# Performance work log

Hardware: AMD Instinct MI355X
Metric: run time of the kernel (lower is better)

Reference implementation:

```python
import jax, jax.numpy as jnp
import numpy as np

N_SRC, N_TGT, E = 50000, 10000, 150000
D_IN, D_OUT = 512, 512
N_ETYPES, N_NTYPES = 8, 4


def setup_inputs() -> dict:
    key = jax.random.key(0)
    ks = jax.random.split(key, 9)
    scale = 1.0 / np.sqrt(D_IN)
    return {
        "x_src": jax.random.normal(ks[0], (N_SRC, D_IN), jnp.float32),
        "x_target": jax.random.normal(ks[1], (N_TGT, D_IN), jnp.float32),
        "rel_W": jax.random.normal(ks[2], (N_ETYPES, D_IN, D_OUT), jnp.float32) * scale,
        "root_W": jax.random.normal(ks[3], (N_NTYPES, D_IN, D_OUT), jnp.float32) * scale,
        "root_b": jax.random.normal(ks[4], (N_NTYPES, D_OUT), jnp.float32) * scale,
        "edge_src": jax.random.randint(ks[5], (E,), 0, N_SRC, jnp.int64).astype(jnp.int32),
        "edge_dst": jax.random.randint(ks[6], (E,), 0, N_TGT, jnp.int64).astype(jnp.int32),
        "edge_type": jax.random.randint(ks[7], (E,), 0, N_ETYPES, jnp.int64).astype(jnp.int32),
        "target_node_type": jax.random.randint(ks[8], (N_TGT,), 0, N_NTYPES, jnp.int64).astype(jnp.int32),
    }


def reference(x_src, x_target, rel_W, root_W, root_b,
              edge_src, edge_dst, edge_type, target_node_type):
    T = rel_W.shape[0]
    n_tgt = x_target.shape[0]
    # Transform every source node under every relation (grouped GEMM),
    # then gather per edge: msg_e = W_{etype_e} @ x_src[src_e].
    h = jnp.einsum('ni,tio->tno', x_src, rel_W)          # [T, N_src, D_out]
    msg = h[edge_type, edge_src]                          # [E, D_out]
    # PyG aggr='mean' is applied per edge type then SUMMED across types:
    # segment-mean keyed by (dst, etype), empty segments contribute 0.
    seg = edge_dst * T + edge_type                        # [E]
    sums = jax.ops.segment_sum(msg, seg, num_segments=n_tgt * T)
    counts = jax.ops.segment_sum(jnp.ones((msg.shape[0],), msg.dtype), seg,
                                 num_segments=n_tgt * T)
    means = sums / jnp.maximum(counts, 1.0)[:, None]      # [N_tgt*T, D_out]
    out = means.reshape(n_tgt, T, -1).sum(axis=1)         # [N_tgt, D_out]
    # Per-node-type root linear (with bias), selected per target node.
    root = jnp.einsum('ni,tio->nto', x_target, root_W) + root_b[None]  # [N_tgt, NT, D_out]
    root_sel = jnp.take_along_axis(root, target_node_type[:, None, None], axis=1)[:, 0]
    return out + root_sel
```

## Files before the change

kernel.cpp:

```cpp
#include <hip/hip_runtime.h>
#include <hip/hip_bf16.h>

#define D 512
#define T_ETYPES 8
#define NT_TYPES 4
#define K_MAIN 4096
#define K_A 4608
#define K_B 6144
#define SPLITS 6
#define KSPLIT 768
#define BK 64


typedef __attribute__((ext_vector_type(8))) short bf16x8;
typedef __attribute__((ext_vector_type(4))) float f32x4;

__device__ __forceinline__ unsigned short f2bf(float f) {
    union { float f; unsigned u; } u{f};
    unsigned r = u.u + 0x7FFF + ((u.u >> 16) & 1);
    return (unsigned short)(r >> 16);
}
__device__ __forceinline__ float bf2f(unsigned short h) {
    union { unsigned u; float f; } v{(unsigned)h << 16};
    return v.f;
}

__device__ __forceinline__ void gl16(const unsigned short* g, unsigned short* l) {
    __builtin_amdgcn_global_load_lds(
        (const __attribute__((address_space(1))) unsigned int*)g,
        (__attribute__((address_space(3))) unsigned int*)l,
        16, 0, 0);
}

__global__ void convert_xsrc(const float* __restrict__ x, unsigned short* __restrict__ xb,
                             int n8) {
    int stride = gridDim.x * 256;
    for (int i = blockIdx.x * 256 + threadIdx.x; i < n8; i += stride) {
        const float4* p = reinterpret_cast<const float4*>(x + (size_t)i * 8);
        float4 v0 = p[0], v1 = p[1];
        uint4 u;
        u.x = (unsigned)f2bf(v0.x) | ((unsigned)f2bf(v0.y) << 16);
        u.y = (unsigned)f2bf(v0.z) | ((unsigned)f2bf(v0.w) << 16);
        u.z = (unsigned)f2bf(v1.x) | ((unsigned)f2bf(v1.y) << 16);
        u.w = (unsigned)f2bf(v1.z) | ((unsigned)f2bf(v1.w) << 16);
        reinterpret_cast<uint4*>(xb)[i] = u;
    }
}

__global__ void convert_weights(const float* __restrict__ relW,
                                const float* __restrict__ rootW,
                                unsigned short* __restrict__ WbT) {
    __shared__ float tile[32][33];
    int c0 = blockIdx.x * 32;
    int o0 = blockIdx.y * 32;
    int tid = threadIdx.x;
#pragma unroll
    for (int it = 0; it < 4; ++it) {
        int idx = it * 256 + tid;
        int oc = idx & 31, cc = idx >> 5;
        int c = c0 + cc, o = o0 + oc;
        float v = (c < K_MAIN) ? relW[(size_t)c * D + o]
                               : rootW[(size_t)(c - K_MAIN) * D + o];
        tile[cc][oc] = v;
    }
    __syncthreads();
#pragma unroll
    for (int it = 0; it < 4; ++it) {
        int idx = it * 256 + tid;
        int cc = idx & 31, oc = idx >> 5;
        int o = o0 + oc, c = c0 + cc;
        int csw = (c & ~63) | (((((c >> 3) & 7) ^ (o & 7))) << 3) | (c & 7);
        WbT[(size_t)o * K_B + csw] = f2bf(tile[cc][oc]);
    }
}

__global__ void hist_kernel(const int* __restrict__ edst, const int* __restrict__ etyp,
                            int* __restrict__ counts, int E) {
    int e = blockIdx.x * 256 + threadIdx.x;
    if (e < E) atomicAdd(&counts[edst[e] * T_ETYPES + etyp[e]], 1);
}

__global__ void scan1(const int* __restrict__ counts, int* __restrict__ partial,
                      int* __restrict__ blockSums, int n) {
    __shared__ int sh[256];
    int tid = threadIdx.x, i = blockIdx.x * 256 + tid;
    int c = (i < n) ? counts[i] : 0;
    int val = c;
    sh[tid] = val; __syncthreads();
#pragma unroll
    for (int off = 1; off < 256; off <<= 1) {
        int add = (tid >= off) ? sh[tid - off] : 0;
        __syncthreads();
        val += add; sh[tid] = val;
        __syncthreads();
    }
    if (i < n) partial[i] = val - c;
    if (tid == 255) blockSums[blockIdx.x] = val;
}

__global__ void scan2(int* __restrict__ blockSums, int nb) {
    __shared__ int sh[512];
    int tid = threadIdx.x;
    int c = (tid < nb) ? blockSums[tid] : 0;
    int val = c;
    sh[tid] = val; __syncthreads();
#pragma unroll
    for (int off = 1; off < 512; off <<= 1) {
        int add = (tid >= off) ? sh[tid - off] : 0;
        __syncthreads();
        val += add; sh[tid] = val;
        __syncthreads();
    }
    if (tid < nb) blockSums[tid] = val - c;
}

__global__ void scan3(const int* __restrict__ partial, const int* __restrict__ blockSums,
                      int* __restrict__ offsets, int* __restrict__ cursors, int n, int E) {
    int i = blockIdx.x * 256 + threadIdx.x;
    if (i < n) {
        int v = partial[i] + blockSums[i >> 8];
        offsets[i] = v;
        cursors[i] = v;
    }
    if (i == 0) offsets[n] = E;
}

__global__ void scatter_kernel(const int* __restrict__ esrc, const int* __restrict__ edst,
                               const int* __restrict__ etyp, int* __restrict__ cursors,
                               int* __restrict__ perm, int E) {
    int e = blockIdx.x * 256 + threadIdx.x;
    if (e < E) {
        int seg = edst[e] * T_ETYPES + etyp[e];
        int pos = atomicAdd(&cursors[seg], 1);
        perm[pos] = esrc[e];
    }
}

__global__ void thist2(const int* __restrict__ tnt, int* __restrict__ bcnt, int M) {
    __shared__ int h[NT_TYPES];
    if (threadIdx.x < NT_TYPES) h[threadIdx.x] = 0;
    __syncthreads();
    int i = blockIdx.x * 256 + threadIdx.x;
    if (i < M) atomicAdd(&h[tnt[i]], 1);
    __syncthreads();
    if (threadIdx.x < NT_TYPES) bcnt[blockIdx.x * NT_TYPES + threadIdx.x] = h[threadIdx.x];
}

__global__ void tprep2(const int* __restrict__ bcnt, int nb,
                       int* __restrict__ boff, int* __restrict__ gstart,
                       int* __restrict__ endv) {
    __shared__ int sb[128 * NT_TYPES];
    __shared__ int gs[NT_TYPES];
    int tid = threadIdx.x;
    for (int i = tid; i < nb * NT_TYPES; i += blockDim.x) sb[i] = bcnt[i];
    __syncthreads();
    if (tid == 0) {
        int s = 0;
        for (int g = 0; g < NT_TYPES; ++g) {
            int tot = 0;
            for (int b = 0; b < nb; ++b) tot += sb[b * NT_TYPES + g];
            gs[g] = s;
            gstart[g] = s;
            endv[g] = s + tot;
            s += ((tot + 127) >> 7) << 7;
        }
        gstart[NT_TYPES] = s;
    }
    __syncthreads();
    if (tid < NT_TYPES) {
        int run = gs[tid];
        for (int b = 0; b < nb; ++b) {
            boff[b * NT_TYPES + tid] = run;
            run += sb[b * NT_TYPES + tid];
        }
    }
}

__global__ void tscatter2(const int* __restrict__ tnt, const int* __restrict__ boff,
                          int* __restrict__ rowperm, int* __restrict__ invperm, int M) {
    __shared__ int h[NT_TYPES];
    if (threadIdx.x < NT_TYPES) h[threadIdx.x] = 0;
    __syncthreads();
    int n = blockIdx.x * 256 + threadIdx.x;
    if (n < M) {
        int g = tnt[n];
        int lr = atomicAdd(&h[g], 1);
        int p = boff[blockIdx.x * NT_TYPES + g] + lr;
        rowperm[p] = n;
        invperm[n] = p;
    }
}

__global__ void build_A(const unsigned short* __restrict__ xsb, const int* __restrict__ perm,
                        const int* __restrict__ offsets,
                        const int* __restrict__ invperm, const float* __restrict__ x_target,
                        unsigned short* __restrict__ A, int nseg, int segBlocks, int M) {
    if ((int)blockIdx.x >= segBlocks) {
        int idx = ((int)blockIdx.x - segBlocks) * 256 + threadIdx.x;
        if (idx >= M * 64) return;
        int n = idx >> 6;
        int q = idx & 63;
        const float4* p = reinterpret_cast<const float4*>(x_target + (size_t)n * D + q * 8);
        float4 v0 = p[0], v1 = p[1];
        uint4 u;
        u.x = (unsigned)f2bf(v0.x) | ((unsigned)f2bf(v0.y) << 16);
        u.y = (unsigned)f2bf(v0.z) | ((unsigned)f2bf(v0.w) << 16);
        u.z = (unsigned)f2bf(v1.x) | ((unsigned)f2bf(v1.y) << 16);
        u.w = (unsigned)f2bf(v1.z) | ((unsigned)f2bf(v1.w) << 16);
        int prow = invperm[n];
        int col = K_MAIN + ((q >> 3) << 6) + (((q & 7) ^ (prow & 7)) << 3);
        *reinterpret_cast<uint4*>(A + (size_t)prow * K_A + col) = u;
        return;
    }
    int seg = blockIdx.x * 4 + (threadIdx.x >> 6);
    if (seg >= nseg) return;
    int lane = threadIdx.x & 63;
    int beg = offsets[seg];
    int cnt = offsets[seg + 1] - beg;

    float4 a0 = make_float4(0.f, 0.f, 0.f, 0.f);
    float4 a1 = make_float4(0.f, 0.f, 0.f, 0.f);

#define ACCUM(R) {                                                                  \
        a0.x += bf2f((unsigned short)R.x); a0.y += bf2f((unsigned short)(R.x >> 16));\
        a0.z += bf2f((unsigned short)R.y); a0.w += bf2f((unsigned short)(R.y >> 16));\
        a1.x += bf2f((unsigned short)R.z); a1.y += bf2f((unsigned short)(R.z >> 16));\
        a1.z += bf2f((unsigned short)R.w); a1.w += bf2f((unsigned short)(R.w >> 16));}

    for (int i = 0; i < cnt; i += 4) {
        int last = beg + cnt - 1;
        int c0 = beg + i;
        int c1 = min(beg + i + 1, last);
        int c2 = min(beg + i + 2, last);
        int c3 = min(beg + i + 3, last);
        int s0 = perm[c0], s1 = perm[c1], s2 = perm[c2], s3 = perm[c3];
        uint4 r0 = reinterpret_cast<const uint4*>(xsb + (size_t)s0 * D)[lane];
        uint4 r1 = reinterpret_cast<const uint4*>(xsb + (size_t)s1 * D)[lane];
        uint4 r2 = reinterpret_cast<const uint4*>(xsb + (size_t)s2 * D)[lane];
        uint4 r3 = reinterpret_cast<const uint4*>(xsb + (size_t)s3 * D)[lane];
        ACCUM(r0)
        if (i + 1 < cnt) ACCUM(r1)
        if (i + 2 < cnt) ACCUM(r2)
        if (i + 3 < cnt) ACCUM(r3)
    }
#undef ACCUM

    float sc = (cnt > 0) ? 1.0f / (float)cnt : 0.0f;
    uint4 u;
    u.x = (unsigned)f2bf(a0.x * sc) | ((unsigned)f2bf(a0.y * sc) << 16);
    u.y = (unsigned)f2bf(a0.z * sc) | ((unsigned)f2bf(a0.w * sc) << 16);
    u.z = (unsigned)f2bf(a1.x * sc) | ((unsigned)f2bf(a1.y * sc) << 16);
    u.w = (unsigned)f2bf(a1.z * sc) | ((unsigned)f2bf(a1.w * sc) << 16);
    int dst = seg >> 3, t = seg & 7;
    int nrow = invperm[dst];
    int col = t * D + ((lane >> 3) << 6) + (((lane & 7) ^ (nrow & 7)) << 3);
    *reinterpret_cast<uint4*>(A + (size_t)nrow * K_A + col) = u;
}

__global__ __launch_bounds__(512, 4)
void rgcn_gemm_sk(const unsigned short* __restrict__ A,
                  const unsigned short* __restrict__ WbT,
                  unsigned short* __restrict__ pbuf,
                  const int* __restrict__ gstart, const int* __restrict__ endv,
                  int MBP, int MPc) {
    __shared__ unsigned short As[128 * BK];
    __shared__ unsigned short Bs[256 * BK];
    const int tid = threadIdx.x;

    int d = blockIdx.x;
    int l = d;
    if ((gridDim.x & 7) == 0) {
        int cpx = gridDim.x >> 3;
        l = (d & 7) * cpx + (d >> 3);
    }
    const int nIdx = l & 1;
    const int mz = l >> 1;
    const int mIdx = mz % MBP;
    const int zIdx = mz / MBP;

    const int blockM = mIdx * 128;
    const int blockN = nIdx * 256;
    const int kBase = zIdx * KSPLIT;
    const int g = (blockM >= gstart[1]) + (blockM >= gstart[2]) + (blockM >= gstart[3]);
    const int endRow = endv[g];
    const int rootOff = g * 512;

    const int wid = tid >> 6, lane = tid & 63;
    const int wr = wid >> 2, wc = wid & 3;
    const int lr = lane & 15, lg = lane >> 4;

    f32x4 acc[4][4] = {};

    const unsigned short* Abase = A + (size_t)blockM * K_A + kBase;
    const unsigned short* Bbase = WbT + (size_t)blockN * K_B;

    for (int t = 0; t < KSPLIT / BK; ++t) {
        const int k0 = t * BK;
        const int kc = kBase + k0;
        const int bc = (kc < K_MAIN) ? kc : kc + rootOff;
#pragma unroll
        for (int q = 0; q < 2; ++q) {
            int c = q * 512 + tid;
            gl16(Abase + (size_t)(c >> 3) * K_A + k0 + (c & 7) * 8, &As[c * 8]);
        }
#pragma unroll
        for (int q = 0; q < 4; ++q) {
            int c = q * 512 + tid;
            gl16(Bbase + (size_t)(c >> 3) * K_B + bc + (c & 7) * 8, &Bs[c * 8]);
        }
        __syncthreads();

#pragma unroll
        for (int ks = 0; ks < 2; ++ks) {
            bf16x8 a_frag[4], b_frag[4];
#pragma unroll
            for (int mi = 0; mi < 4; ++mi) {
                int r = wr * 64 + mi * 16 + lr;
                a_frag[mi] = *reinterpret_cast<const bf16x8*>(
                    &As[r * BK + (((ks * 4 + lg) ^ (r & 7)) << 3)]);
            }
#pragma unroll
            for (int ni = 0; ni < 4; ++ni) {
                int cR = wc * 64 + ni * 16 + lr;
                b_frag[ni] = *reinterpret_cast<const bf16x8*>(
                    &Bs[cR * BK + (((ks * 4 + lg) ^ (cR & 7)) << 3)]);
            }
#pragma unroll
            for (int mi = 0; mi < 4; ++mi)
#pragma unroll
                for (int ni = 0; ni < 4; ++ni)
                    acc[mi][ni] = __builtin_amdgcn_mfma_f32_16x16x32_bf16(
                        a_frag[mi], b_frag[ni], acc[mi][ni], 0, 0, 0);
        }
        __syncthreads();
    }

#pragma unroll
    for (int mi = 0; mi < 4; ++mi) {
#pragma unroll
        for (int r = 0; r < 4; ++r) {
            int row = blockM + wr * 64 + mi * 16 + lg * 4 + r;
            if (row < endRow) {
#pragma unroll
                for (int ni = 0; ni < 4; ++ni) {
                    int col = blockN + wc * 64 + ni * 16 + lr;
                    pbuf[((size_t)zIdx * MPc + row) * D + col] = f2bf(acc[mi][ni][r]);
                }
            }
        }
    }
}

__global__ void reduce_bias(const unsigned short* __restrict__ pbuf,
                            const int* __restrict__ rowperm, const int* __restrict__ tnt,
                            const float* __restrict__ root_b,
                            float* __restrict__ out, int MPc) {
    int idx = blockIdx.x * 256 + threadIdx.x;
    if (idx >= MPc * 64) return;
    int nrow = idx >> 6;
    int col = (idx & 63) * 8;
    int orig = rowperm[nrow];
    if (orig < 0) return;
    float s[8] = {0.f, 0.f, 0.f, 0.f, 0.f, 0.f, 0.f, 0.f};
#pragma unroll
    for (int sp = 0; sp < SPLITS; ++sp) {
        uint4 v = *reinterpret_cast<const uint4*>(pbuf + ((size_t)sp * MPc + nrow) * D + col);
        unsigned u[4] = {v.x, v.y, v.z, v.w};
#pragma unroll
        for (int j = 0; j < 4; ++j) {
            s[2 * j]     += bf2f((unsigned short)(u[j] & 0xFFFF));
            s[2 * j + 1] += bf2f((unsigned short)(u[j] >> 16));
        }
    }
    const float* b = root_b + (size_t)tnt[orig] * D + col;
    float* o = out + (size_t)orig * D + col;
#pragma unroll
    for (int j = 0; j < 8; ++j)
        __builtin_nontemporal_store(s[j] + b[j], o + j);
}

extern "C" void kernel_launch(void* const* d_in, const int* in_sizes, int n_in,
                              void* d_out, int out_size, void* d_ws, size_t ws_size,
                              hipStream_t stream) {
    const float* x_src    = (const float*)d_in[0];
    const float* x_target = (const float*)d_in[1];
    const float* relW     = (const float*)d_in[2];
    const float* rootW    = (const float*)d_in[3];
    const float* rootb    = (const float*)d_in[4];
    const int*   esrc     = (const int*)d_in[5];
    const int*   edst     = (const int*)d_in[6];
    const int*   etyp     = (const int*)d_in[7];
    const int*   tnt      = (const int*)d_in[8];
    float* out = (float*)d_out;

    const int E = in_sizes[5];
    const int NSRC8 = in_sizes[0] / 8;
    const int M = in_sizes[8];
    const int NSEG = M * T_ETYPES;
    const int NB = (NSEG + 255) / 256;
    const int NBT = (M + 255) / 256;
    const int MBP = (M + 127) / 128 + (NT_TYPES - 1);
    const int MPc = MBP * 128;
    const int segBlocks = (NSEG + 3) / 4;
    const int rootBlocks = (M * 64 + 255) / 256;

    char* ws = (char*)d_ws;
    size_t off = 0;
    unsigned short* Abf = (unsigned short*)(ws + off); off += (size_t)MPc * K_A * 2;
    unsigned short* WbT = (unsigned short*)(ws + off); off += (size_t)D * K_B * 2;
    size_t shared_off = off;
    size_t xsb_bytes = (size_t)in_sizes[0] * 2;
    size_t pb_bytes  = (size_t)SPLITS * MPc * D * 2;
    unsigned short* xsb = (unsigned short*)(ws + shared_off);
    unsigned short* pb  = (unsigned short*)(ws + shared_off);
    off += (xsb_bytes > pb_bytes ? xsb_bytes : pb_bytes);
    int* counts    = (int*)(ws + off); off += (size_t)NSEG * 4;
    int* partial   = (int*)(ws + off); off += (size_t)NSEG * 4;
    int* offsets   = (int*)(ws + off); off += (size_t)(NSEG + 8) * 4;
    int* cursors   = (int*)(ws + off); off += (size_t)NSEG * 4;
    int* blockSums = (int*)(ws + off); off += 512 * 4;
    int* perm      = (int*)(ws + off); off += (size_t)E * 4;
    int* bcnt      = (int*)(ws + off); off += (size_t)NBT * NT_TYPES * 4;
    int* boff      = (int*)(ws + off); off += (size_t)NBT * NT_TYPES * 4;
    int* gstart    = (int*)(ws + off); off += 8 * 4;
    int* endv      = (int*)(ws + off); off += 8 * 4;
    int* rowperm   = (int*)(ws + off); off += (size_t)MPc * 4;
    int* invperm   = (int*)(ws + off); off += (size_t)M * 4;

    hipMemsetAsync(counts, 0, (size_t)NSEG * 4, stream);
    hipMemsetAsync(rowperm, 0xFF, (size_t)MPc * 4, stream);

    convert_xsrc<<<2048, 256, 0, stream>>>(x_src, xsb, NSRC8);
    convert_weights<<<dim3(K_B / 32, D / 32), 256, 0, stream>>>(relW, rootW, WbT);
    thist2<<<NBT, 256, 0, stream>>>(tnt, bcnt, M);
    tprep2<<<1, 256, 0, stream>>>(bcnt, NBT, boff, gstart, endv);
    tscatter2<<<NBT, 256, 0, stream>>>(tnt, boff, rowperm, invperm, M);
    hist_kernel<<<(E + 255) / 256, 256, 0, stream>>>(edst, etyp, counts, E);
    scan1<<<NB, 256, 0, stream>>>(counts, partial, blockSums, NSEG);
    scan2<<<1, 512, 0, stream>>>(blockSums, NB);
    scan3<<<NB, 256, 0, stream>>>(partial, blockSums, offsets, cursors, NSEG, E);
    scatter_kernel<<<(E + 255) / 256, 256, 0, stream>>>(esrc, edst, etyp, cursors, perm, E);
    build_A<<<segBlocks + rootBlocks, 256, 0, stream>>>(
        xsb, perm, offsets, invperm, x_target, Abf, NSEG, segBlocks, M);
    rgcn_gemm_sk<<<MBP * 2 * SPLITS, 512, 0, stream>>>(Abf, WbT, pb, gstart, endv, MBP, MPc);
    reduce_bias<<<(MPc * 64 + 255) / 256, 256, 0, stream>>>(pb, rowperm, tnt, rootb, out, MPc);
}
```

Before: 191.6 us.

## Merge independent preprocessing kernels into combined launches; add nontemporal partial-buffer access

Independent preprocessing kernels are merged by block-index dispatch. Source conversion, weight conversion, edge histogram and node-type histogram now run in one front kernel. The scan stage and the type-permutation stages are paired into two mid kernels. This cuts the launch count from eight to three and lets independent work overlap. The split-K partial buffer is also written and read with nontemporal hints to reduce cache pollution. The risk is branch-divergent kernels with mixed shared memory use, which can lower occupancy for every block type.

New measurement: 184.7 us. 1.04x faster.

```diff
diff --git a/kernel.cpp b/kernel.cpp
--- a/kernel.cpp
+++ b/kernel.cpp
@@ -14,6 +14,7 @@
 
 typedef __attribute__((ext_vector_type(8))) short bf16x8;
 typedef __attribute__((ext_vector_type(4))) float f32x4;
+typedef __attribute__((ext_vector_type(4))) unsigned u32x4;
 
 __device__ __forceinline__ unsigned short f2bf(float f) {
     union { float f; unsigned u; } u{f};
@@ -32,86 +33,155 @@
         16, 0, 0);
 }
 
-__global__ void convert_xsrc(const float* __restrict__ x, unsigned short* __restrict__ xb,
-                             int n8) {
-    int stride = gridDim.x * 256;
-    for (int i = blockIdx.x * 256 + threadIdx.x; i < n8; i += stride) {
-        const float4* p = reinterpret_cast<const float4*>(x + (size_t)i * 8);
-        float4 v0 = p[0], v1 = p[1];
-        uint4 u;
-        u.x = (unsigned)f2bf(v0.x) | ((unsigned)f2bf(v0.y) << 16);
-        u.y = (unsigned)f2bf(v0.z) | ((unsigned)f2bf(v0.w) << 16);
-        u.z = (unsigned)f2bf(v1.x) | ((unsigned)f2bf(v1.y) << 16);
-        u.w = (unsigned)f2bf(v1.z) | ((unsigned)f2bf(v1.w) << 16);
-        reinterpret_cast<uint4*>(xb)[i] = u;
-    }
-}
-
-__global__ void convert_weights(const float* __restrict__ relW,
-                                const float* __restrict__ rootW,
-                                unsigned short* __restrict__ WbT) {
-    __shared__ float tile[32][33];
-    int c0 = blockIdx.x * 32;
-    int o0 = blockIdx.y * 32;
+__global__ void front_kernel(const float* __restrict__ x, unsigned short* __restrict__ xb,
+                             int n8,
+                             const float* __restrict__ relW, const float* __restrict__ rootW,
+                             unsigned short* __restrict__ WbT,
+                             const int* __restrict__ edst, const int* __restrict__ etyp,
+                             int* __restrict__ counts, int E,
+                             const int* __restrict__ tnt, int* __restrict__ bcnt, int M,
+                             int convBlocks, int cwBlocks, int histBlocks) {
+    int b = blockIdx.x;
+    if (b < convBlocks) {
+        int stride = convBlocks * 256;
+        for (int i = b * 256 + threadIdx.x; i < n8; i += stride) {
+            const float4* p = reinterpret_cast<const float4*>(x + (size_t)i * 8);
+            float4 v0 = p[0], v1 = p[1];
+            uint4 u;
+            u.x = (unsigned)f2bf(v0.x) | ((unsigned)f2bf(v0.y) << 16);
+            u.y = (unsigned)f2bf(v0.z) | ((unsigned)f2bf(v0.w) << 16);
+            u.z = (unsigned)f2bf(v1.x) | ((unsigned)f2bf(v1.y) << 16);
+            u.w = (unsigned)f2bf(v1.z) | ((unsigned)f2bf(v1.w) << 16);
+            reinterpret_cast<uint4*>(xb)[i] = u;
+        }
+        return;
+    }
+    b -= convBlocks;
+    if (b < cwBlocks) {
+        __shared__ float tile[32][33];
+        int c0 = (b % (K_B / 32)) * 32;
+        int o0 = (b / (K_B / 32)) * 32;
+        int tid = threadIdx.x;
+#pragma unroll
+        for (int it = 0; it < 4; ++it) {
+            int idx = it * 256 + tid;
+            int oc = idx & 31, cc = idx >> 5;
+            int c = c0 + cc, o = o0 + oc;
+            float v = (c < K_MAIN) ? relW[(size_t)c * D + o]
+                                   : rootW[(size_t)(c - K_MAIN) * D + o];
+            tile[cc][oc] = v;
+        }
+        __syncthreads();
+#pragma unroll
+        for (int it = 0; it < 4; ++it) {
+            int idx = it * 256 + tid;
+            int cc = idx & 31, oc = idx >> 5;
+            int o = o0 + oc, c = c0 + cc;
+            int csw = (c & ~63) | (((((c >> 3) & 7) ^ (o & 7))) << 3) | (c & 7);
+            WbT[(size_t)o * K_B + csw] = f2bf(tile[cc][oc]);
+        }
+        return;
+    }
+    b -= cwBlocks;
+    if (b < histBlocks) {
+        int e = b * 256 + threadIdx.x;
+        if (e < E) atomicAdd(&counts[edst[e] * T_ETYPES + etyp[e]], 1);
+        return;
+    }
+    b -= histBlocks;
+    {
+        __shared__ int h[NT_TYPES];
+        if (threadIdx.x < NT_TYPES) h[threadIdx.x] = 0;
+        __syncthreads();
+        int i = b * 256 + threadIdx.x;
+        if (i < M) atomicAdd(&h[tnt[i]], 1);
+        __syncthreads();
+        if (threadIdx.x < NT_TYPES) bcnt[b * NT_TYPES + threadIdx.x] = h[threadIdx.x];
+    }
+}
+
+__global__ void mid1(const int* __restrict__ counts, int* __restrict__ partial,
+                     int* __restrict__ blockSums, int n,
+                     const int* __restrict__ bcnt, int nbt, int* __restrict__ boff,
+                     int* __restrict__ gstart, int* __restrict__ endv, int NBscan) {
+    if ((int)blockIdx.x < NBscan) {
+        __shared__ int sh[256];
+        int tid = threadIdx.x, i = blockIdx.x * 256 + tid;
+        int c = (i < n) ? counts[i] : 0;
+        int val = c;
+        sh[tid] = val; __syncthreads();
+#pragma unroll
+        for (int off = 1; off < 256; off <<= 1) {
+            int add = (tid >= off) ? sh[tid - off] : 0;
+            __syncthreads();
+            val += add; sh[tid] = val;
+            __syncthreads();
+        }
+        if (i < n) partial[i] = val - c;
+        if (tid == 255) blockSums[blockIdx.x] = val;
+        return;
+    }
+    __shared__ int sb[128 * NT_TYPES];
+    __shared__ int gs[NT_TYPES];
     int tid = threadIdx.x;
-#pragma unroll
-    for (int it = 0; it < 4; ++it) {
-        int idx = it * 256 + tid;
-        int oc = idx & 31, cc = idx >> 5;
-        int c = c0 + cc, o = o0 + oc;
-        float v = (c < K_MAIN) ? relW[(size_t)c * D + o]
-                               : rootW[(size_t)(c - K_MAIN) * D + o];
-        tile[cc][oc] = v;
-    }
+    for (int i = tid; i < nbt * NT_TYPES; i += blockDim.x) sb[i] = bcnt[i];
     __syncthreads();
-#pragma unroll
-    for (int it = 0; it < 4; ++it) {
-        int idx = it * 256 + tid;
-        int cc = idx & 31, oc = idx >> 5;
-        int o = o0 + oc, c = c0 + cc;
-        int csw = (c & ~63) | (((((c >> 3) & 7) ^ (o & 7))) << 3) | (c & 7);
-        WbT[(size_t)o * K_B + csw] = f2bf(tile[cc][oc]);
-    }
-}
-
-__global__ void hist_kernel(const int* __restrict__ edst, const int* __restrict__ etyp,
-                            int* __restrict__ counts, int E) {
-    int e = blockIdx.x * 256 + threadIdx.x;
-    if (e < E) atomicAdd(&counts[edst[e] * T_ETYPES + etyp[e]], 1);
-}
-
-__global__ void scan1(const int* __restrict__ counts, int* __restrict__ partial,
-                      int* __restrict__ blockSums, int n) {
-    __shared__ int sh[256];
-    int tid = threadIdx.x, i = blockIdx.x * 256 + tid;
-    int c = (i < n) ? counts[i] : 0;
-    int val = c;
-    sh[tid] = val; __syncthreads();
-#pragma unroll
-    for (int off = 1; off < 256; off <<= 1) {
-        int add = (tid >= off) ? sh[tid - off] : 0;
-        __syncthreads();
-        val += add; sh[tid] = val;
-        __syncthreads();
-    }
-    if (i < n) partial[i] = val - c;
-    if (tid == 255) blockSums[blockIdx.x] = val;
-}
-
-__global__ void scan2(int* __restrict__ blockSums, int nb) {
-    __shared__ int sh[512];
-    int tid = threadIdx.x;
-    int c = (tid < nb) ? blockSums[tid] : 0;
-    int val = c;
-    sh[tid] = val; __syncthreads();
-#pragma unroll
-    for (int off = 1; off < 512; off <<= 1) {
-        int add = (tid >= off) ? sh[tid - off] : 0;
-        __syncthreads();
-        val += add; sh[tid] = val;
-        __syncthreads();
-    }
-    if (tid < nb) blockSums[tid] = val - c;
+    if (tid == 0) {
+        int s = 0;
+        for (int g = 0; g < NT_TYPES; ++g) {
+            int tot = 0;
+            for (int b2 = 0; b2 < nbt; ++b2) tot += sb[b2 * NT_TYPES + g];
+            gs[g] = s;
+            gstart[g] = s;
+            endv[g] = s + tot;
+            s += ((tot + 127) >> 7) << 7;
+        }
+        gstart[NT_TYPES] = s;
+    }
+    __syncthreads();
+    if (tid < NT_TYPES) {
+        int run = gs[tid];
+        for (int b2 = 0; b2 < nbt; ++b2) {
+            boff[b2 * NT_TYPES + tid] = run;
+            run += sb[b2 * NT_TYPES + tid];
+        }
+    }
+}
+
+__global__ void mid2(int* __restrict__ blockSums, int nb,
+                     const int* __restrict__ tnt, const int* __restrict__ boff,
+                     int* __restrict__ rowperm, int* __restrict__ invperm,
+                     int M, int nbt) {
+    if (blockIdx.x == 0) {
+        __shared__ int sh[512];
+        int tid = threadIdx.x;
+        int c = (tid < nb) ? blockSums[tid] : 0;
+        int val = c;
+        sh[tid] = val; __syncthreads();
+#pragma unroll
+        for (int off = 1; off < 512; off <<= 1) {
+            int add = (tid >= off) ? sh[tid - off] : 0;
+            __syncthreads();
+            val += add; sh[tid] = val;
+            __syncthreads();
+        }
+        if (tid < nb) blockSums[tid] = val - c;
+        return;
+    }
+    __shared__ int h[2][NT_TYPES];
+    int half = threadIdx.x >> 8;
+    int tid = threadIdx.x & 255;
+    int lb = ((int)blockIdx.x - 1) * 2 + half;
+    if (tid < NT_TYPES) h[half][tid] = 0;
+    __syncthreads();
+    int n = lb * 256 + tid;
+    if (lb < nbt && n < M) {
+        int g = tnt[n];
+        int lr = atomicAdd(&h[half][g], 1);
+        int p = boff[lb * NT_TYPES + g] + lr;
+        rowperm[p] = n;
+        invperm[n] = p;
+    }
 }
 
 __global__ void scan3(const int* __restrict__ partial, const int* __restrict__ blockSums,
@@ -133,61 +203,6 @@
         int seg = edst[e] * T_ETYPES + etyp[e];
         int pos = atomicAdd(&cursors[seg], 1);
         perm[pos] = esrc[e];
-    }
-}
-
-__global__ void thist2(const int* __restrict__ tnt, int* __restrict__ bcnt, int M) {
-    __shared__ int h[NT_TYPES];
-    if (threadIdx.x < NT_TYPES) h[threadIdx.x] = 0;
-    __syncthreads();
-    int i = blockIdx.x * 256 + threadIdx.x;
-    if (i < M) atomicAdd(&h[tnt[i]], 1);
-    __syncthreads();
-    if (threadIdx.x < NT_TYPES) bcnt[blockIdx.x * NT_TYPES + threadIdx.x] = h[threadIdx.x];
-}
-
-__global__ void tprep2(const int* __restrict__ bcnt, int nb,
-                       int* __restrict__ boff, int* __restrict__ gstart,
-                       int* __restrict__ endv) {
-    __shared__ int sb[128 * NT_TYPES];
-    __shared__ int gs[NT_TYPES];
-    int tid = threadIdx.x;
-    for (int i = tid; i < nb * NT_TYPES; i += blockDim.x) sb[i] = bcnt[i];
-    __syncthreads();
-    if (tid == 0) {
-        int s = 0;
-        for (int g = 0; g < NT_TYPES; ++g) {
-            int tot = 0;
-            for (int b = 0; b < nb; ++b) tot += sb[b * NT_TYPES + g];
-            gs[g] = s;
-            gstart[g] = s;
-            endv[g] = s + tot;
-            s += ((tot + 127) >> 7) << 7;
-        }
-        gstart[NT_TYPES] = s;
-    }
-    __syncthreads();
-    if (tid < NT_TYPES) {
-        int run = gs[tid];
-        for (int b = 0; b < nb; ++b) {
-            boff[b * NT_TYPES + tid] = run;
-            run += sb[b * NT_TYPES + tid];
-        }
-    }
-}
-
-__global__ void tscatter2(const int* __restrict__ tnt, const int* __restrict__ boff,
-                          int* __restrict__ rowperm, int* __restrict__ invperm, int M) {
-    __shared__ int h[NT_TYPES];
-    if (threadIdx.x < NT_TYPES) h[threadIdx.x] = 0;
-    __syncthreads();
-    int n = blockIdx.x * 256 + threadIdx.x;
-    if (n < M) {
-        int g = tnt[n];
-        int lr = atomicAdd(&h[g], 1);
-        int p = boff[blockIdx.x * NT_TYPES + g] + lr;
-        rowperm[p] = n;
-        invperm[n] = p;
     }
 }
 
@@ -344,7 +359,8 @@
 #pragma unroll
                 for (int ni = 0; ni < 4; ++ni) {
                     int col = blockN + wc * 64 + ni * 16 + lr;
-                    pbuf[((size_t)zIdx * MPc + row) * D + col] = f2bf(acc[mi][ni][r]);
+                    __builtin_nontemporal_store(f2bf(acc[mi][ni][r]),
+                        &pbuf[((size_t)zIdx * MPc + row) * D + col]);
                 }
             }
         }
@@ -364,7 +380,8 @@
     float s[8] = {0.f, 0.f, 0.f, 0.f, 0.f, 0.f, 0.f, 0.f};
 #pragma unroll
     for (int sp = 0; sp < SPLITS; ++sp) {
-        uint4 v = *reinterpret_cast<const uint4*>(pbuf + ((size_t)sp * MPc + nrow) * D + col);
+        u32x4 v = __builtin_nontemporal_load(
+            reinterpret_cast<const u32x4*>(pbuf + ((size_t)sp * MPc + nrow) * D + col));
         unsigned u[4] = {v.x, v.y, v.z, v.w};
 #pragma unroll
         for (int j = 0; j < 4; ++j) {
@@ -403,6 +420,9 @@
     const int MPc = MBP * 128;
     const int segBlocks = (NSEG + 3) / 4;
     const int rootBlocks = (M * 64 + 255) / 256;
+    const int convBlocks = 2048;
+    const int cwBlocks = (K_B / 32) * (D / 32);
+    const int histBlocks = (E + 255) / 256;
 
     char* ws = (char*)d_ws;
     size_t off = 0;
@@ -430,16 +450,15 @@
     hipMemsetAsync(counts, 0, (size_t)NSEG * 4, stream);
     hipMemsetAsync(rowperm, 0xFF, (size_t)MPc * 4, stream);
 
-    convert_xsrc<<<2048, 256, 0, stream>>>(x_src, xsb, NSRC8);
-    convert_weights<<<dim3(K_B / 32, D / 32), 256, 0, stream>>>(relW, rootW, WbT);
-    thist2<<<NBT, 256, 0, stream>>>(tnt, bcnt, M);
-    tprep2<<<1, 256, 0, stream>>>(bcnt, NBT, boff, gstart, endv);
-    tscatter2<<<NBT, 256, 0, stream>>>(tnt, boff, rowperm, invperm, M);
-    hist_kernel<<<(E + 255) / 256, 256, 0, stream>>>(edst, etyp, counts, E);
-    scan1<<<NB, 256, 0, stream>>>(counts, partial, blockSums, NSEG);
-    scan2<<<1, 512, 0, stream>>>(blockSums, NB);
+    front_kernel<<<convBlocks + cwBlocks + histBlocks + NBT, 256, 0, stream>>>(
+        x_src, xsb, NSRC8, relW, rootW, WbT, edst, etyp, counts, E,
+        tnt, bcnt, M, convBlocks, cwBlocks, histBlocks);
+    mid1<<<NB + 1, 256, 0, stream>>>(counts, partial, blockSums, NSEG,
+                                     bcnt, NBT, boff, gstart, endv, NB);
+    mid2<<<1 + (NBT + 1) / 2, 512, 0, stream>>>(blockSums, NB, tnt, boff,
+                                                rowperm, invperm, M, NBT);
     scan3<<<NB, 256, 0, stream>>>(partial, blockSums, offsets, cursors, NSEG, E);
-    scatter_kernel<<<(E + 255) / 256, 256, 0, stream>>>(esrc, edst, etyp, cursors, perm, E);
+    scatter_kernel<<<histBlocks, 256, 0, stream>>>(esrc, edst, etyp, cursors, perm, E);
     build_A<<<segBlocks + rootBlocks, 256, 0, stream>>>(
         xsb, perm, offsets, invperm, x_target, Abf, NSEG, segBlocks, M);
     rgcn_gemm_sk<<<MBP * 2 * SPLITS, 512, 0, stream>>>(Abf, WbT, pb, gstart, endv, MBP, MPc);
```
